# Kernel optimization log

Hardware: AMD Instinct MI355X
Metric: run time of the kernel (lower is better)

The kernel has to match this reference:

```python
import jax, jax.numpy as jnp
import numpy as np

IN_F, OUT_F = 4096, 11008
B, S = 2, 2048

def setup_inputs() -> dict:
    key = jax.random.key(0)
    k1, k2, k3, k4 = jax.random.split(key, 4)
    x = jax.random.normal(k1, (B, S, IN_F), dtype=jnp.float32)
    # int8 quantized weight, stored as int8 buffer [out_features, in_features]
    w8 = jax.random.randint(k2, (OUT_F, IN_F), -128, 128, dtype=jnp.int32).astype(jnp.int8)
    scales = jax.random.normal(k3, (OUT_F,), dtype=jnp.float32)
    bias = jax.random.normal(k4, (1, OUT_F), dtype=jnp.float32)
    return {"input": x, "int8_weights": w8, "scales": scales, "bias": bias}

def reference(input, int8_weights, scales, bias):
    # w8_a16_forward: cast int8 weight to activation dtype, dense GEMM,
    # then per-output-channel scale and bias add.
    w = int8_weights.astype(input.dtype)                 # [OUT_F, IN_F]
    y = jnp.einsum('bsi,oi->bso', input, w)              # [B, S, OUT_F]
    return y * scales + bias                             # scales broadcast over last dim; bias [1, OUT_F]
```

## Files before the change

### kernel.cpp

```cpp
#include <hip/hip_runtime.h>
#include <stdint.h>

#define MM 4096
#define KK 4096
#define NN 11008

typedef __bf16 bf16;
typedef bf16 bf16x8 __attribute__((ext_vector_type(8)));
typedef float f32x4 __attribute__((ext_vector_type(4)));

static_assert(sizeof(bf16x8) == 16, "bf16x8 must be 16B");

__device__ __forceinline__ void async_ld16(const void* g, void* l) {
  __builtin_amdgcn_global_load_lds(
      (const __attribute__((address_space(1))) uint32_t*)g,
      (__attribute__((address_space(3))) uint32_t*)l,
      16, 0, 0);
}

__global__ __launch_bounds__(256) void cvt_a_kernel(const float* __restrict__ in,
                                                    bf16* __restrict__ out, int n4) {
  int i = blockIdx.x * 256 + threadIdx.x;
  if (i >= n4) return;
  float4 v = ((const float4*)in)[i];
  union { bf16 h[4]; uint2 u; } p;
  p.h[0] = (bf16)v.x; p.h[1] = (bf16)v.y; p.h[2] = (bf16)v.z; p.h[3] = (bf16)v.w;
  ((uint2*)out)[i] = p.u;
}

__global__ __launch_bounds__(256) void cvt_w_kernel(const int* __restrict__ in,
                                                    bf16* __restrict__ out, int n4) {
  int i = blockIdx.x * 256 + threadIdx.x;
  if (i >= n4) return;
  int4 v = ((const int4*)in)[i];
  union { bf16 h[4]; uint2 u; } p;
  p.h[0] = (bf16)(float)v.x; p.h[1] = (bf16)(float)v.y;
  p.h[2] = (bf16)(float)v.z; p.h[3] = (bf16)(float)v.w;
  ((uint2*)out)[i] = p.u;
}

__device__ __forceinline__ void mfma_step(const bf16* As, const bf16* Ws,
                                          int lane, int wr, int wc, f32x4 acc[4][4]) {
  const int m16 = lane & 15;
  const int k   = lane >> 4;
  const int jj  = (k + (m16 >> 1)) & 3;
  bf16x8 af[4], bg[4];
#pragma unroll
  for (int t = 0; t < 4; ++t) {
    af[t] = *(const bf16x8*)(As + (wr * 64 + t * 16 + m16) * 32 + jj * 8);
    bg[t] = *(const bf16x8*)(Ws + (wc * 64 + t * 16 + m16) * 32 + jj * 8);
  }
#pragma unroll
  for (int tm = 0; tm < 4; ++tm)
#pragma unroll
    for (int tn = 0; tn < 4; ++tn)
      acc[tm][tn] = __builtin_amdgcn_mfma_f32_16x16x32_bf16(af[tm], bg[tn], acc[tm][tn], 0, 0, 0);
}

__device__ __forceinline__ void epilogue(f32x4 acc[4][4],
                                         const float* __restrict__ scales,
                                         const float* __restrict__ bias,
                                         float* __restrict__ out,
                                         int bm, int bn, int lane, int wr, int wc) {
  const int row0 = bm * 128 + wr * 64 + ((lane >> 4) * 4);
  const int col0 = bn * 128 + wc * 64 + (lane & 15);
#pragma unroll
  for (int tn = 0; tn < 4; ++tn) {
    const int col = col0 + tn * 16;
    const float s = scales[col];
    const float b = bias[col];
#pragma unroll
    for (int tm = 0; tm < 4; ++tm) {
      const int r0 = row0 + tm * 16;
#pragma unroll
      for (int r = 0; r < 4; ++r)
        out[(long)(r0 + r) * NN + col] = acc[tm][tn][r] * s + b;
    }
  }
}

__global__ __launch_bounds__(256, 2) void gemm_bf16_kernel(
    const bf16* __restrict__ A,
    const bf16* __restrict__ W,
    const float* __restrict__ scales,
    const float* __restrict__ bias,
    float* __restrict__ out) {
  __shared__ bf16 As[128 * 32];
  __shared__ bf16 Ws[128 * 32];
  const int tid  = threadIdx.x;
  const int lane = tid & 63;
  const int wave = tid >> 6;
  const int wr   = wave >> 1, wc = wave & 1;
  const int bm   = blockIdx.x, bn = blockIdx.y;

  f32x4 acc[4][4] = {};

  const bf16* Ab = A + (long)bm * 128 * KK;
  const bf16* Wb = W + (long)bn * 128 * KK;

  for (int k0 = 0; k0 < KK; k0 += 32) {
    __syncthreads();
#pragma unroll
    for (int j2 = 0; j2 < 2; ++j2) {
      const int c = j2 * 256 + tid;
      const int r = c >> 2;
      const int j = c & 3;
      const int k = (j - (r >> 1)) & 3;
      const long goff = (long)r * KK + k0 + k * 8;
      async_ld16(Ab + goff, As + j2 * 2048 + wave * 512);
      async_ld16(Wb + goff, Ws + j2 * 2048 + wave * 512);
    }
    __syncthreads();
    mfma_step(As, Ws, lane, wr, wc, acc);
  }
  epilogue(acc, scales, bias, out, bm, bn, lane, wr, wc);
}

__global__ __launch_bounds__(256, 2) void gemm_fused_kernel(
    const float* __restrict__ A,
    const int* __restrict__ W32,
    const float* __restrict__ scales,
    const float* __restrict__ bias,
    float* __restrict__ out) {
  __shared__ bf16 As[128 * 32];
  __shared__ bf16 Ws[128 * 32];
  const int tid  = threadIdx.x;
  const int lane = tid & 63;
  const int wave = tid >> 6;
  const int wr   = wave >> 1, wc = wave & 1;
  const int bm   = blockIdx.x, bn = blockIdx.y;

  f32x4 acc[4][4] = {};

  const int r    = tid >> 1;
  const int kk16 = (tid & 1) * 16;

  const float* Ag = A + (long)(bm * 128 + r) * KK + kk16;
  const int*   Wg = W32 + (long)(bn * 128 + r) * KK + kk16;
  bf16* Asw = As + r * 32 + kk16;
  bf16* Wsw = Ws + r * 32 + kk16;

  for (int k0 = 0; k0 < KK; k0 += 32) {
    float4 a0 = *(const float4*)(Ag + k0);
    float4 a1 = *(const float4*)(Ag + k0 + 4);
    float4 a2 = *(const float4*)(Ag + k0 + 8);
    float4 a3 = *(const float4*)(Ag + k0 + 12);
    int4 v0 = *(const int4*)(Wg + k0);
    int4 v1 = *(const int4*)(Wg + k0 + 4);
    int4 v2 = *(const int4*)(Wg + k0 + 8);
    int4 v3 = *(const int4*)(Wg + k0 + 12);
    __syncthreads();
    bf16x8 h0, h1, w0, w1;
    h0[0] = (bf16)a0.x; h0[1] = (bf16)a0.y; h0[2] = (bf16)a0.z; h0[3] = (bf16)a0.w;
    h0[4] = (bf16)a1.x; h0[5] = (bf16)a1.y; h0[6] = (bf16)a1.z; h0[7] = (bf16)a1.w;
    h1[0] = (bf16)a2.x; h1[1] = (bf16)a2.y; h1[2] = (bf16)a2.z; h1[3] = (bf16)a2.w;
    h1[4] = (bf16)a3.x; h1[5] = (bf16)a3.y; h1[6] = (bf16)a3.z; h1[7] = (bf16)a3.w;
    w0[0] = (bf16)(float)v0.x; w0[1] = (bf16)(float)v0.y;
    w0[2] = (bf16)(float)v0.z; w0[3] = (bf16)(float)v0.w;
    w0[4] = (bf16)(float)v1.x; w0[5] = (bf16)(float)v1.y;
    w0[6] = (bf16)(float)v1.z; w0[7] = (bf16)(float)v1.w;
    w1[0] = (bf16)(float)v2.x; w1[1] = (bf16)(float)v2.y;
    w1[2] = (bf16)(float)v2.z; w1[3] = (bf16)(float)v2.w;
    w1[4] = (bf16)(float)v3.x; w1[5] = (bf16)(float)v3.y;
    w1[6] = (bf16)(float)v3.z; w1[7] = (bf16)(float)v3.w;
    *(bf16x8*)(Asw)     = h0;
    *(bf16x8*)(Asw + 8) = h1;
    *(bf16x8*)(Wsw)     = w0;
    *(bf16x8*)(Wsw + 8) = w1;
    __syncthreads();
    const int m16 = lane & 15;
    const int ko  = (lane >> 4) * 8;
    bf16x8 af[4], bg[4];
#pragma unroll
    for (int t = 0; t < 4; ++t) {
      af[t] = *(const bf16x8*)(As + (wr * 64 + t * 16 + m16) * 32 + ko);
      bg[t] = *(const bf16x8*)(Ws + (wc * 64 + t * 16 + m16) * 32 + ko);
    }
#pragma unroll
    for (int tm = 0; tm < 4; ++tm)
#pragma unroll
      for (int tn = 0; tn < 4; ++tn)
        acc[tm][tn] = __builtin_amdgcn_mfma_f32_16x16x32_bf16(af[tm], bg[tn], acc[tm][tn], 0, 0, 0);
  }
  epilogue(acc, scales, bias, out, bm, bn, lane, wr, wc);
}

extern "C" void kernel_launch(void* const* d_in, const int* in_sizes, int n_in,
                              void* d_out, int out_size, void* d_ws, size_t ws_size,
                              hipStream_t stream) {
  const float* x      = (const float*)d_in[0];
  const int*   w32    = (const int*)d_in[1];
  const float* scales = (const float*)d_in[2];
  const float* bias   = (const float*)d_in[3];
  float*       out    = (float*)d_out;

  const size_t A_BYTES = (size_t)MM * KK * 2;
  const size_t W_BYTES = (size_t)NN * KK * 2;
  dim3 grid(MM / 128, NN / 128);

  if (ws_size >= A_BYTES + W_BYTES) {
    bf16* A16 = (bf16*)d_ws;
    bf16* W16 = (bf16*)((char*)d_ws + A_BYTES);
    const int na = MM * KK / 4;
    hipLaunchKernelGGL(cvt_a_kernel, dim3((na + 255) / 256), dim3(256), 0, stream, x, A16, na);
    const int nw = NN * KK / 4;
    hipLaunchKernelGGL(cvt_w_kernel, dim3((nw + 255) / 256), dim3(256), 0, stream, w32, W16, nw);
    hipLaunchKernelGGL(gemm_bf16_kernel, grid, dim3(256), 0, stream, A16, W16, scales, bias, out);
  } else {
    hipLaunchKernelGGL(gemm_fused_kernel, grid, dim3(256), 0, stream, x, w32, scales, bias, out);
  }
}
```

Baseline: 739.2 us.

## Replace 128x128 bf16 GEMM with 256x256 double-buffered, pipelined 8-wave kernel

Swaps the 128x128 single-buffered GEMM for a 256x256 tile computed by 512 threads with 64-wide K chunks. It double-buffers LDS with async global-to-LDS loads staged in halves between four MFMA phases, uses s_setprio and swizzled LDS addressing, and remaps blocks for L2 locality. The aim is higher arithmetic intensity and overlap of loads with MFMA work. In exchange it uses 128KB of dynamic LDS, which limits occupancy, plus heavy register pressure from 32 accumulators per thread.

New measurement: 698.6 us. 1.06x faster.

```diff
diff --git a/kernel.cpp b/kernel.cpp
--- a/kernel.cpp
+++ b/kernel.cpp
@@ -4,6 +4,7 @@
 #define MM 4096
 #define KK 4096
 #define NN 11008
+#define NK 64
 
 typedef __bf16 bf16;
 typedef bf16 bf16x8 __attribute__((ext_vector_type(8)));
@@ -39,81 +40,181 @@
   ((uint2*)out)[i] = p.u;
 }
 
-__device__ __forceinline__ void mfma_step(const bf16* As, const bf16* Ws,
-                                          int lane, int wr, int wc, f32x4 acc[4][4]) {
-  const int m16 = lane & 15;
-  const int k   = lane >> 4;
-  const int jj  = (k + (m16 >> 1)) & 3;
-  bf16x8 af[4], bg[4];
-#pragma unroll
-  for (int t = 0; t < 4; ++t) {
-    af[t] = *(const bf16x8*)(As + (wr * 64 + t * 16 + m16) * 32 + jj * 8);
-    bg[t] = *(const bf16x8*)(Ws + (wc * 64 + t * 16 + m16) * 32 + jj * 8);
-  }
-#pragma unroll
-  for (int tm = 0; tm < 4; ++tm)
-#pragma unroll
-    for (int tn = 0; tn < 4; ++tn)
-      acc[tm][tn] = __builtin_amdgcn_mfma_f32_16x16x32_bf16(af[tm], bg[tn], acc[tm][tn], 0, 0, 0);
-}
-
-__device__ __forceinline__ void epilogue(f32x4 acc[4][4],
-                                         const float* __restrict__ scales,
-                                         const float* __restrict__ bias,
-                                         float* __restrict__ out,
-                                         int bm, int bn, int lane, int wr, int wc) {
-  const int row0 = bm * 128 + wr * 64 + ((lane >> 4) * 4);
-  const int col0 = bn * 128 + wc * 64 + (lane & 15);
-#pragma unroll
-  for (int tn = 0; tn < 4; ++tn) {
-    const int col = col0 + tn * 16;
-    const float s = scales[col];
-    const float b = bias[col];
-#pragma unroll
-    for (int tm = 0; tm < 4; ++tm) {
-      const int r0 = row0 + tm * 16;
-#pragma unroll
-      for (int r = 0; r < 4; ++r)
-        out[(long)(r0 + r) * NN + col] = acc[tm][tn][r] * s + b;
-    }
-  }
-}
-
-__global__ __launch_bounds__(256, 2) void gemm_bf16_kernel(
+__global__ __launch_bounds__(512, 2) void gemm256_kernel(
     const bf16* __restrict__ A,
     const bf16* __restrict__ W,
     const float* __restrict__ scales,
     const float* __restrict__ bias,
     float* __restrict__ out) {
-  __shared__ bf16 As[128 * 32];
-  __shared__ bf16 Ws[128 * 32];
+  extern __shared__ bf16 lds[];
+  bf16* LA = lds;
+  bf16* LB = lds + 2 * 16384;
+
   const int tid  = threadIdx.x;
   const int lane = tid & 63;
   const int wave = tid >> 6;
-  const int wr   = wave >> 1, wc = wave & 1;
-  const int bm   = blockIdx.x, bn = blockIdx.y;
-
-  f32x4 acc[4][4] = {};
-
-  const bf16* Ab = A + (long)bm * 128 * KK;
-  const bf16* Wb = W + (long)bn * 128 * KK;
-
-  for (int k0 = 0; k0 < KK; k0 += 32) {
-    __syncthreads();
-#pragma unroll
-    for (int j2 = 0; j2 < 2; ++j2) {
-      const int c = j2 * 256 + tid;
-      const int r = c >> 2;
-      const int j = c & 3;
-      const int k = (j - (r >> 1)) & 3;
-      const long goff = (long)r * KK + k0 + k * 8;
-      async_ld16(Ab + goff, As + j2 * 2048 + wave * 512);
-      async_ld16(Wb + goff, Ws + j2 * 2048 + wave * 512);
+  const int wr   = wave >> 2;
+  const int wc   = wave & 3;
+
+  const int flat = blockIdx.y * 16 + blockIdx.x;
+  const int swz  = (flat & 7) * 86 + (flat >> 3);
+  const int bm   = swz & 15;
+  const int bn   = swz >> 4;
+
+  const int t2   = (tid & 32) ? (tid ^ 2) : tid;
+  const int srow = tid >> 3;
+  const int skel = (t2 & 7) * 8;
+  const bf16* gA = A + (size_t)(bm * 256 + srow) * KK + skel;
+  const bf16* gW = W + (size_t)(bn * 256 + srow) * KK + skel;
+
+  const int m16  = lane & 15;
+  const int kk   = ((lane >> 4) * 8) ^ (((lane >> 2) & 1) * 16);
+  const int aRow = wr * 128 + m16;
+  const int bRow = wc * 64 + m16;
+
+  f32x4 acc[8][4] = {};
+
+  auto stage_half = [&](const bf16* g, bf16* l) {
+    async_ld16(g, l + wave * 512);
+    async_ld16(g + (size_t)64 * KK, l + 64 * 64 + wave * 512);
+  };
+  stage_half(gW,                    LB);
+  stage_half(gA,                    LA);
+  stage_half(gW + (size_t)128 * KK, LB + 128 * 64);
+  stage_half(gA + (size_t)128 * KK, LA + 128 * 64);
+  stage_half(gW + 64,               LB + 16384);
+  stage_half(gA + 64,               LA + 16384);
+  asm volatile("s_waitcnt vmcnt(4)" ::: "memory");
+  __builtin_amdgcn_s_barrier();
+
+  for (int c = 0; c < NK; ++c) {
+    const int cb = c & 1;
+    const bf16* At = LA + cb * 16384;
+    const bf16* Wt = LB + cb * 16384;
+    bf16* An = LA + (cb ^ 1) * 16384;
+    bf16* Bn = LB + (cb ^ 1) * 16384;
+    bf16* Ac = LA + cb * 16384;
+    bf16* Bc = LB + cb * 16384;
+    const size_t k1 = (size_t)(c + 1) * 64;
+    const size_t k2 = (size_t)(c + 2) * 64;
+
+    bf16x8 aLo[4][2], aHi[4][2], bLo[2][2], bHi[2][2];
+
+#pragma unroll
+    for (int fm = 0; fm < 4; ++fm)
+#pragma unroll
+      for (int kc = 0; kc < 2; ++kc)
+        aLo[fm][kc] = *(const bf16x8*)(At + (aRow + fm * 16) * 64 + kc * 32 + kk);
+#pragma unroll
+    for (int fn = 0; fn < 2; ++fn)
+#pragma unroll
+      for (int kc = 0; kc < 2; ++kc)
+        bLo[fn][kc] = *(const bf16x8*)(Wt + (bRow + fn * 16) * 64 + kc * 32 + kk);
+    if (c + 1 < NK) stage_half(gW + (size_t)128 * KK + k1, Bn + 128 * 64);
+    __builtin_amdgcn_s_barrier();
+    asm volatile("s_waitcnt lgkmcnt(0)" ::: "memory");
+    __builtin_amdgcn_s_setprio(1);
+#pragma unroll
+    for (int fm = 0; fm < 4; ++fm)
+#pragma unroll
+      for (int fn = 0; fn < 2; ++fn)
+#pragma unroll
+        for (int kc = 0; kc < 2; ++kc)
+          acc[fm][fn] = __builtin_amdgcn_mfma_f32_16x16x32_bf16(aLo[fm][kc], bLo[fn][kc], acc[fm][fn], 0, 0, 0);
+    __builtin_amdgcn_s_setprio(0);
+    __builtin_amdgcn_s_barrier();
+
+#pragma unroll
+    for (int fn = 0; fn < 2; ++fn)
+#pragma unroll
+      for (int kc = 0; kc < 2; ++kc)
+        bHi[fn][kc] = *(const bf16x8*)(Wt + (bRow + (fn + 2) * 16) * 64 + kc * 32 + kk);
+    if (c + 1 < NK) stage_half(gA + (size_t)128 * KK + k1, An + 128 * 64);
+    __builtin_amdgcn_s_barrier();
+    asm volatile("s_waitcnt lgkmcnt(0)" ::: "memory");
+    __builtin_amdgcn_s_setprio(1);
+#pragma unroll
+    for (int fm = 0; fm < 4; ++fm)
+#pragma unroll
+      for (int fn = 0; fn < 2; ++fn)
+#pragma unroll
+        for (int kc = 0; kc < 2; ++kc)
+          acc[fm][fn + 2] = __builtin_amdgcn_mfma_f32_16x16x32_bf16(aLo[fm][kc], bHi[fn][kc], acc[fm][fn + 2], 0, 0, 0);
+    __builtin_amdgcn_s_setprio(0);
+    __builtin_amdgcn_s_barrier();
+
+#pragma unroll
+    for (int fm = 0; fm < 4; ++fm)
+#pragma unroll
+      for (int kc = 0; kc < 2; ++kc)
+        aHi[fm][kc] = *(const bf16x8*)(At + (aRow + (fm + 4) * 16) * 64 + kc * 32 + kk);
+    if (c + 2 < NK) stage_half(gW + k2, Bc);
+    __builtin_amdgcn_s_barrier();
+    asm volatile("s_waitcnt lgkmcnt(0)" ::: "memory");
+    __builtin_amdgcn_s_setprio(1);
+#pragma unroll
+    for (int fm = 0; fm < 4; ++fm)
+#pragma unroll
+      for (int fn = 0; fn < 2; ++fn)
+#pragma unroll
+        for (int kc = 0; kc < 2; ++kc)
+          acc[fm + 4][fn] = __builtin_amdgcn_mfma_f32_16x16x32_bf16(aHi[fm][kc], bLo[fn][kc], acc[fm + 4][fn], 0, 0, 0);
+    __builtin_amdgcn_s_setprio(0);
+    __builtin_amdgcn_s_barrier();
+
+    if (c + 2 < NK) stage_half(gA + k2, Ac);
+    __builtin_amdgcn_s_barrier();
+    __builtin_amdgcn_s_setprio(1);
+#pragma unroll
+    for (int fm = 0; fm < 4; ++fm)
+#pragma unroll
+      for (int fn = 0; fn < 2; ++fn)
+#pragma unroll
+        for (int kc = 0; kc < 2; ++kc)
+          acc[fm + 4][fn + 2] = __builtin_amdgcn_mfma_f32_16x16x32_bf16(aHi[fm][kc], bHi[fn][kc], acc[fm + 4][fn + 2], 0, 0, 0);
+    __builtin_amdgcn_s_setprio(0);
+    if (c + 2 < NK) asm volatile("s_waitcnt vmcnt(4)" ::: "memory");
+    else            asm volatile("s_waitcnt vmcnt(0)" ::: "memory");
+    __builtin_amdgcn_s_barrier();
+  }
+
+  const int row0 = bm * 256 + wr * 128 + ((lane >> 4) * 4);
+  const int col0 = bn * 256 + wc * 64 + (lane & 15);
+#pragma unroll
+  for (int fn = 0; fn < 4; ++fn) {
+    const int col = col0 + fn * 16;
+    const float s = scales[col];
+    const float b = bias[col];
+#pragma unroll
+    for (int fm = 0; fm < 8; ++fm) {
+      const int r0 = row0 + fm * 16;
+#pragma unroll
+      for (int r = 0; r < 4; ++r)
+        out[(size_t)(r0 + r) * NN + col] = acc[fm][fn][r] * s + b;
     }
-    __syncthreads();
-    mfma_step(As, Ws, lane, wr, wc, acc);
-  }
-  epilogue(acc, scales, bias, out, bm, bn, lane, wr, wc);
+  }
+}
+
+__device__ __forceinline__ void epilogue128(f32x4 acc[4][4],
+                                            const float* __restrict__ scales,
+                                            const float* __restrict__ bias,
+                                            float* __restrict__ out,
+                                            int bm, int bn, int lane, int wr, int wc) {
+  const int row0 = bm * 128 + wr * 64 + ((lane >> 4) * 4);
+  const int col0 = bn * 128 + wc * 64 + (lane & 15);
+#pragma unroll
+  for (int tn = 0; tn < 4; ++tn) {
+    const int col = col0 + tn * 16;
+    const float s = scales[col];
+    const float b = bias[col];
+#pragma unroll
+    for (int tm = 0; tm < 4; ++tm) {
+      const int r0 = row0 + tm * 16;
+#pragma unroll
+      for (int r = 0; r < 4; ++r)
+        out[(long)(r0 + r) * NN + col] = acc[tm][tn][r] * s + b;
+    }
+  }
 }
 
 __global__ __launch_bounds__(256, 2) void gemm_fused_kernel(
@@ -182,7 +283,7 @@
       for (int tn = 0; tn < 4; ++tn)
         acc[tm][tn] = __builtin_amdgcn_mfma_f32_16x16x32_bf16(af[tm], bg[tn], acc[tm][tn], 0, 0, 0);
   }
-  epilogue(acc, scales, bias, out, bm, bn, lane, wr, wc);
+  epilogue128(acc, scales, bias, out, bm, bn, lane, wr, wc);
 }
 
 extern "C" void kernel_launch(void* const* d_in, const int* in_sizes, int n_in,
@@ -196,17 +297,24 @@
 
   const size_t A_BYTES = (size_t)MM * KK * 2;
   const size_t W_BYTES = (size_t)NN * KK * 2;
-  dim3 grid(MM / 128, NN / 128);
 
   if (ws_size >= A_BYTES + W_BYTES) {
+    static bool attr_done = false;
+    if (!attr_done) {
+      (void)hipFuncSetAttribute((const void*)gemm256_kernel,
+                                hipFuncAttributeMaxDynamicSharedMemorySize, 131072);
+      attr_done = true;
+    }
     bf16* A16 = (bf16*)d_ws;
     bf16* W16 = (bf16*)((char*)d_ws + A_BYTES);
     const int na = MM * KK / 4;
     hipLaunchKernelGGL(cvt_a_kernel, dim3((na + 255) / 256), dim3(256), 0, stream, x, A16, na);
     const int nw = NN * KK / 4;
     hipLaunchKernelGGL(cvt_w_kernel, dim3((nw + 255) / 256), dim3(256), 0, stream, w32, W16, nw);
-    hipLaunchKernelGGL(gemm_bf16_kernel, grid, dim3(256), 0, stream, A16, W16, scales, bias, out);
+    hipLaunchKernelGGL(gemm256_kernel, dim3(MM / 256, NN / 256), dim3(512), 131072, stream,
+                       A16, W16, scales, bias, out);
   } else {
-    hipLaunchKernelGGL(gemm_fused_kernel, grid, dim3(256), 0, stream, x, w32, scales, bias, out);
-  }
-}
+    hipLaunchKernelGGL(gemm_fused_kernel, dim3(MM / 128, NN / 128), dim3(256), 0, stream,
+                       x, w32, scales, bias, out);
+  }
+}
```
